# Performance work log

Measured on AMD Instinct MI355X. Metric: run time of the kernel, lower is better.

Reference implementation:

```python
import jax, jax.numpy as jnp
import numpy as np
import math

D_MODEL = 1024
N_HEADS = 16
D_K = D_MODEL // N_HEADS
FFN = 4096
B, S = 4, 1024
EPS = 1e-5


def setup_inputs() -> dict:
    key = jax.random.key(0)
    ks = jax.random.split(key, 24)
    sd = 0.02
    def w(k, shape):
        return jax.random.normal(k, shape, dtype=jnp.float32) * sd
    inp = {
        'x': jax.random.normal(ks[0], (B, S, D_MODEL), dtype=jnp.float32),
        'enc': jax.random.normal(ks[1], (B, S, D_MODEL), dtype=jnp.float32),
        'mask': jnp.tril(jnp.ones((S, S), dtype=jnp.int32)),  # causal look-ahead mask
        # stacked per-head projections [H, d_model, d_k], biases [H, d_k]
        'Wq_self': w(ks[2], (N_HEADS, D_MODEL, D_K)), 'bq_self': w(ks[3], (N_HEADS, D_K)),
        'Wk_self': w(ks[4], (N_HEADS, D_MODEL, D_K)), 'bk_self': w(ks[5], (N_HEADS, D_K)),
        'Wv_self': w(ks[6], (N_HEADS, D_MODEL, D_K)), 'bv_self': w(ks[7], (N_HEADS, D_K)),
        'Wq_x': w(ks[8], (N_HEADS, D_MODEL, D_K)), 'bq_x': w(ks[9], (N_HEADS, D_K)),
        'Wk_x': w(ks[10], (N_HEADS, D_MODEL, D_K)), 'bk_x': w(ks[11], (N_HEADS, D_K)),
        'Wv_x': w(ks[12], (N_HEADS, D_MODEL, D_K)), 'bv_x': w(ks[13], (N_HEADS, D_K)),
        # W_O is SHARED between self- and cross-attention (as in the torch code)
        'Wo': w(ks[14], (D_MODEL, D_MODEL)), 'bo': w(ks[15], (D_MODEL,)),
        'W1': w(ks[16], (D_MODEL, FFN)), 'b1': w(ks[17], (FFN,)),
        'W2': w(ks[18], (FFN, D_MODEL)), 'b2': w(ks[19], (D_MODEL,)),
        'g1': jnp.ones((D_MODEL,), jnp.float32), 'be1': jnp.zeros((D_MODEL,), jnp.float32),
        'g2': jnp.ones((D_MODEL,), jnp.float32), 'be2': jnp.zeros((D_MODEL,), jnp.float32),
        'g3': jnp.ones((D_MODEL,), jnp.float32), 'be3': jnp.zeros((D_MODEL,), jnp.float32),
    }
    return inp


def _layernorm(x, g, b):
    mu = jnp.mean(x, axis=-1, keepdims=True)
    d = x - mu
    var = jnp.mean(d * d, axis=-1, keepdims=True)
    return d * jax.lax.rsqrt(var + EPS) * g + b


def _mha(xq, xkv, Wq, bq, Wk, bk, Wv, bv, mask):
    # batched equivalent of the per-head Python loop
    q = jnp.einsum('bsd,hdk->bhsk', xq, Wq) + bq[None, :, None, :]
    k = jnp.einsum('btd,hdk->bhtk', xkv, Wk) + bk[None, :, None, :]
    v = jnp.einsum('btd,hdk->bhtk', xkv, Wv) + bv[None, :, None, :]
    scores = jnp.einsum('bhsk,bhtk->bhst', q, k) / math.sqrt(D_K)
    if mask is not None:
        scores = jnp.where(mask[None, None] == 0, -jnp.inf, scores)
    attn = jax.nn.softmax(scores, axis=-1)
    z = jnp.einsum('bhst,bhtk->bhsk', attn, v)
    # concat heads along last dim (head i occupies slice i, matching torch.cat)
    b_, h_, s_, k_ = z.shape
    return jnp.transpose(z, (0, 2, 1, 3)).reshape(b_, s_, h_ * k_)


def reference(x, enc, mask, Wq_self, bq_self, Wk_self, bk_self, Wv_self, bv_self,
              Wq_x, bq_x, Wk_x, bk_x, Wv_x, bv_x, Wo, bo, W1, b1, W2, b2,
              g1, be1, g2, be2, g3, be3):
    sa = _mha(x, x, Wq_self, bq_self, Wk_self, bk_self, Wv_self, bv_self, mask)
    x1 = _layernorm(x + sa @ Wo + bo, g1, be1)
    ca = _mha(x1, enc, Wq_x, bq_x, Wk_x, bk_x, Wv_x, bv_x, None)
    x2 = _layernorm(x1 + ca @ Wo + bo, g2, be2)
    ffn = jax.nn.relu(x2 @ W1 + b1) @ W2 + b2
    return _layernorm(x2 + ffn, g3, be3)
```

## Files before the change

### kernel.cpp

```cpp
#include <hip/hip_runtime.h>
#include <cstdint>

typedef __bf16 bf16_t;
typedef bf16_t bf16x8 __attribute__((ext_vector_type(8)));
typedef bf16_t bf16x4 __attribute__((ext_vector_type(4)));
typedef float  f32x4  __attribute__((ext_vector_type(4)));

#define DEVI static __device__ __forceinline__

DEVI void async_ld16(const bf16_t* g, bf16_t* l) {
  __builtin_amdgcn_global_load_lds((const __attribute__((address_space(1))) void*)g,
                                   (__attribute__((address_space(3))) void*)l, 16, 0, 0);
}

struct PrepArgs {
  const float *WqS, *WkS, *WvS, *WqX, *WkX, *WvX, *Wo, *W1, *W2, *x, *enc;
  const float *bqS, *bkS, *bvS, *bkX, *bvX;
  bf16_t *WqkvST, *WqXT, *WkvXT, *WoT, *W1T, *W2T, *xb, *encb;
  float *bqkv, *bkvx;
};

__global__ __launch_bounds__(256)
void k_prep(PrepArgs a)
{
  __shared__ float tile[32][33];
  const int blk = blockIdx.x, tid = threadIdx.x;
  const int tx = tid & 31, ty = tid >> 5;

  const float* src = nullptr;
  bf16_t* dst = nullptr;
  int srcLd = 0, dstLd = 0, m0 = 0, n0 = 0;
  bool do_tr = false;

  if (blk < 6144) {
    int j = blk >> 10, q = blk & 1023;
    src = j == 0 ? a.WqS : j == 1 ? a.WkS : j == 2 ? a.WvS : j == 3 ? a.WqX : j == 4 ? a.WkX : a.WvX;
    dst = j == 0 ? a.WqkvST : j == 1 ? a.WqkvST + 1048576 : j == 2 ? a.WqkvST + 2097152
        : j == 3 ? a.WqXT : j == 4 ? a.WkvXT : a.WkvXT + 1048576;
    int batch = q >> 6, rem = q & 63;
    src += (long)batch * 65536; dst += (long)batch * 65536;
    srcLd = 64; dstLd = 1024;
    n0 = (rem & 1) * 32; m0 = (rem >> 1) * 32;
    do_tr = true;
  } else if (blk < 7168) {
    int q = blk - 6144;
    src = a.Wo; dst = a.WoT; srcLd = 1024; dstLd = 1024;
    m0 = (q >> 5) * 32; n0 = (q & 31) * 32; do_tr = true;
  } else if (blk < 11264) {
    int q = blk - 7168;
    src = a.W1; dst = a.W1T; srcLd = 4096; dstLd = 1024;
    m0 = (q >> 7) * 32; n0 = (q & 127) * 32; do_tr = true;
  } else if (blk < 15360) {
    int q = blk - 11264;
    src = a.W2; dst = a.W2T; srcLd = 1024; dstLd = 4096;
    m0 = (q >> 5) * 32; n0 = (q & 31) * 32; do_tr = true;
  } else if (blk < 16384) {
    long base = (long)(blk - 15360) * 4096 + tid * 4;
#pragma unroll
    for (int u = 0; u < 4; u++) {
      float4 v = *(const float4*)(a.x + base + u * 1024);
      bf16x4 o; o[0] = (bf16_t)v.x; o[1] = (bf16_t)v.y; o[2] = (bf16_t)v.z; o[3] = (bf16_t)v.w;
      *(bf16x4*)(a.xb + base + u * 1024) = o;
    }
    return;
  } else if (blk < 17408) {
    long base = (long)(blk - 16384) * 4096 + tid * 4;
#pragma unroll
    for (int u = 0; u < 4; u++) {
      float4 v = *(const float4*)(a.enc + base + u * 1024);
      bf16x4 o; o[0] = (bf16_t)v.x; o[1] = (bf16_t)v.y; o[2] = (bf16_t)v.z; o[3] = (bf16_t)v.w;
      *(bf16x4*)(a.encb + base + u * 1024) = o;
    }
    return;
  } else {
    int gi = (blk - 17408) * 1024 + tid * 4;
#pragma unroll
    for (int j = 0; j < 4; j++) {
      int i = gi + j;
      if (i < 1024)      a.bqkv[i] = a.bqS[i];
      else if (i < 2048) a.bqkv[i] = a.bkS[i - 1024];
      else if (i < 3072) a.bqkv[i] = a.bvS[i - 2048];
      else if (i < 4096) a.bkvx[i - 3072] = a.bkX[i - 3072];
      else if (i < 5120) a.bkvx[i - 3072] = a.bvX[i - 4096];
    }
    return;
  }

  if (do_tr) {
#pragma unroll
    for (int i = 0; i < 4; i++)
      tile[ty + i * 8][tx] = src[(long)(m0 + ty + i * 8) * srcLd + n0 + tx];
    __syncthreads();
#pragma unroll
    for (int i = 0; i < 4; i++)
      dst[(long)(n0 + ty + i * 8) * dstLd + m0 + tx] = (bf16_t)tile[tx][ty + i * 8];
  }
}

template<int OUT_MODE, int RELU, int VOFF>
__global__ __launch_bounds__(256, 2)
void k_gemm(const bf16_t* __restrict__ A, int lda,
            const bf16_t* __restrict__ Bt, int ldb,
            const float* __restrict__ bias,
            bf16_t* __restrict__ C, int ldc,
            bf16_t* __restrict__ Vt,
            bf16_t* __restrict__ p0, bf16_t* __restrict__ p1,
            bf16_t* __restrict__ p2, bf16_t* __restrict__ p3,
            int Ktot, int nx)
{
  __shared__ bf16_t As[2][128 * 32];
  __shared__ bf16_t Bs[2][128 * 32];
  const int tid  = threadIdx.x;
  const int wave = tid >> 6, lane = tid & 63;
  const int quad = lane >> 4, m16 = lane & 15;

  int lin = blockIdx.x;
  int perx = gridDim.x >> 3;
  int t = (lin & 7) * perx + (lin >> 3);
  const int bcol = (t % nx) * 128, brow = (t / nx) * 128;
  const int wr = (wave >> 1) * 64, wc = (wave & 1) * 64;

  const int Kper = Ktot / gridDim.z;
  const int k0 = blockIdx.z * Kper;

  f32x4 acc[4][4];
#pragma unroll
  for (int i = 0; i < 4; i++)
#pragma unroll
    for (int j = 0; j < 4; j++) acc[i][j] = (f32x4){0.f, 0.f, 0.f, 0.f};

  auto stage = [&](int kt, int buf) {
#pragma unroll
    for (int i = 0; i < 2; i++) {
      int rg = wave * 2 + i;
      async_ld16(A  + (long)(brow + rg * 16 + m16) * lda + kt + quad * 8, As[buf] + rg * 512);
      async_ld16(Bt + (long)(bcol + rg * 16 + m16) * ldb + kt + quad * 8, Bs[buf] + rg * 512);
    }
  };

  stage(k0, 0);
  __syncthreads();

  const int nIter = Kper >> 5;
  for (int it = 0; it < nIter; it++) {
    const int cur = it & 1;
    if (it + 1 < nIter) stage(k0 + (it + 1) * 32, cur ^ 1);

    bf16x8 af[4], bfr[4];
#pragma unroll
    for (int tt = 0; tt < 4; tt++) {
      af[tt]  = *(const bf16x8*)(As[cur] + ((wr + tt * 16) >> 4) * 512 + quad * 128 + m16 * 8);
      bfr[tt] = *(const bf16x8*)(Bs[cur] + ((wc + tt * 16) >> 4) * 512 + quad * 128 + m16 * 8);
    }
#pragma unroll
    for (int i = 0; i < 4; i++)
#pragma unroll
      for (int j = 0; j < 4; j++)
        acc[i][j] = __builtin_amdgcn_mfma_f32_16x16x32_bf16(af[i], bfr[j], acc[i][j], 0, 0, 0);

    __syncthreads();
  }

  if (OUT_MODE == 1) {
    bf16_t* P = blockIdx.z == 0 ? p0 : blockIdx.z == 1 ? p1 : blockIdx.z == 2 ? p2 : p3;
#pragma unroll
    for (int i = 0; i < 4; i++)
#pragma unroll
      for (int j = 0; j < 4; j++) {
        int col = bcol + wc + j * 16 + m16;
#pragma unroll
        for (int r = 0; r < 4; r++) {
          int row = brow + wr + i * 16 + quad * 4 + r;
          P[(long)row * ldc + col] = (bf16_t)acc[i][j][r];
        }
      }
  } else {
#pragma unroll
    for (int i = 0; i < 4; i++)
#pragma unroll
      for (int j = 0; j < 4; j++) {
        int col = bcol + wc + j * 16 + m16;
        float bv = bias[col];
        if (VOFF && col >= VOFF) {
          int hh = (col - VOFF) >> 6, dd = col & 63;
          int row0 = brow + wr + i * 16 + quad * 4;
          int bb = row0 >> 10, seq = row0 & 1023;
          bf16x4 pk;
#pragma unroll
          for (int r = 0; r < 4; r++) pk[r] = (bf16_t)(acc[i][j][r] + bv);
          *(bf16x4*)(Vt + (long)(bb * 16 + hh) * 65536 + dd * 1024 + seq) = pk;
        } else {
#pragma unroll
          for (int r = 0; r < 4; r++) {
            int row = brow + wr + i * 16 + quad * 4 + r;
            float v = acc[i][j][r] + bv;
            if (RELU) v = v > 0.f ? v : 0.f;
            C[(long)row * ldc + col] = (bf16_t)v;
          }
        }
      }
  }
}

template<int LN, int RESID, int OUTF, int OUTB>
__global__ __launch_bounds__(256)
void k_reduce4(const bf16_t* __restrict__ p0, const bf16_t* __restrict__ p1,
               const bf16_t* __restrict__ p2, const bf16_t* __restrict__ p3,
               const float* __restrict__ bias, const float* __restrict__ resid,
               const float* __restrict__ gamma, const float* __restrict__ beta,
               float* __restrict__ outf, bf16_t* __restrict__ outb)
{
  constexpr int D = 1024;
  __shared__ float red[8];
  int row = blockIdx.x, tid = threadIdx.x;
  long off = (long)row * D + tid * 4;
  bf16x4 a0 = *(const bf16x4*)(p0 + off);
  bf16x4 a1 = *(const bf16x4*)(p1 + off);
  bf16x4 a2 = *(const bf16x4*)(p2 + off);
  bf16x4 a3 = *(const bf16x4*)(p3 + off);
  float4 bb4 = *(const float4*)(bias + tid * 4);
  float4 v;
  v.x = (float)a0[0] + (float)a1[0] + (float)a2[0] + (float)a3[0] + bb4.x;
  v.y = (float)a0[1] + (float)a1[1] + (float)a2[1] + (float)a3[1] + bb4.y;
  v.z = (float)a0[2] + (float)a1[2] + (float)a2[2] + (float)a3[2] + bb4.z;
  v.w = (float)a0[3] + (float)a1[3] + (float)a2[3] + (float)a3[3] + bb4.w;
  if (RESID) {
    float4 q = *(const float4*)(resid + off);
    v.x += q.x; v.y += q.y; v.z += q.z; v.w += q.w;
  }
  float4 y = v;
  if (LN) {
    float s  = v.x + v.y + v.z + v.w;
    float sq = v.x * v.x + v.y * v.y + v.z * v.z + v.w * v.w;
#pragma unroll
    for (int o = 1; o < 64; o <<= 1) {
      s  += __shfl_xor(s, o, 64);
      sq += __shfl_xor(sq, o, 64);
    }
    int wave = tid >> 6, lane = tid & 63;
    if (lane == 0) { red[wave * 2] = s; red[wave * 2 + 1] = sq; }
    __syncthreads();
    float ts = red[0] + red[2] + red[4] + red[6];
    float tq = red[1] + red[3] + red[5] + red[7];
    float mu = ts * (1.f / D);
    float var = tq * (1.f / D) - mu * mu;
    float rstd = rsqrtf(var + 1e-5f);
    float4 g  = *(const float4*)(gamma + tid * 4);
    float4 be = *(const float4*)(beta + tid * 4);
    y.x = (v.x - mu) * rstd * g.x + be.x;
    y.y = (v.y - mu) * rstd * g.y + be.y;
    y.z = (v.z - mu) * rstd * g.z + be.z;
    y.w = (v.w - mu) * rstd * g.w + be.w;
  }
  if (OUTF) *(float4*)(outf + off) = y;
  if (OUTB) {
    bf16x4 o;
    o[0] = (bf16_t)y.x; o[1] = (bf16_t)y.y; o[2] = (bf16_t)y.z; o[3] = (bf16_t)y.w;
    *(bf16x4*)(outb + off) = o;
  }
}

template<int CAUSAL>
__global__ __launch_bounds__(256, 2)
void k_attn(const bf16_t* __restrict__ Q, int ldq,
            const bf16_t* __restrict__ Kp, int ldk,
            const bf16_t* __restrict__ Vt,
            bf16_t* __restrict__ O)
{
  constexpr int S = 1024;
  __shared__ bf16_t Kls[2][4096];
  __shared__ bf16_t Vls[2][4096];
  __shared__ bf16_t Pls[4][32 * 72];

  const int tid = threadIdx.x;
  const int wave = tid >> 6, lane = tid & 63;
  const int quad = lane >> 4, m16 = lane & 15;
  const int qt = blockIdx.x, bh = blockIdx.y, b = bh >> 4, h = bh & 15;
  const int qbase = qt * 128 + wave * 32;

  bf16x8 qf[2][2];
#pragma unroll
  for (int rh = 0; rh < 2; rh++) {
    const bf16_t* qp = Q + (long)(b * S + qbase + rh * 16 + m16) * ldq + h * 64 + quad * 8;
    qf[rh][0] = *(const bf16x8*)qp;
    qf[rh][1] = *(const bf16x8*)(qp + 32);
  }

  f32x4 o_acc[2][4];
#pragma unroll
  for (int rh = 0; rh < 2; rh++)
#pragma unroll
    for (int t = 0; t < 4; t++) o_acc[rh][t] = (f32x4){0.f, 0.f, 0.f, 0.f};
  float rsum[2][4];
#pragma unroll
  for (int rh = 0; rh < 2; rh++)
#pragma unroll
    for (int r = 0; r < 4; r++) rsum[rh][r] = 0.f;

  auto stage = [&](int c, int buf) {
#pragma unroll
    for (int i = 0; i < 2; i++) {
      int t2 = wave * 2 + i;
      int rg = t2 & 3, ph = t2 >> 2;
      async_ld16(Kp + (long)(b * S + c * 64 + rg * 16 + m16) * ldk + h * 64 + ph * 32 + quad * 8,
                 Kls[buf] + t2 * 512);
      async_ld16(Vt + (long)bh * 65536 + (rg * 16 + m16) * 1024 + c * 64 + ph * 32 + quad * 8,
                 Vls[buf] + t2 * 512);
    }
  };

  const int nch = CAUSAL ? (2 * qt + 2) : 16;
  stage(0, 0);

  for (int c = 0; c < nch; c++) {
    __syncthreads();
    const int cur = c & 1;
    if (c + 1 < nch) stage(c + 1, cur ^ 1);

    f32x4 s[2][4];
#pragma unroll
    for (int t = 0; t < 4; t++) {
      bf16x8 k0 = *(const bf16x8*)(Kls[cur] + (0 * 4 + t) * 512 + quad * 128 + m16 * 8);
      bf16x8 k1 = *(const bf16x8*)(Kls[cur] + (1 * 4 + t) * 512 + quad * 128 + m16 * 8);
#pragma unroll
      for (int rh = 0; rh < 2; rh++) {
        f32x4 z = (f32x4){0.f, 0.f, 0.f, 0.f};
        z = __builtin_amdgcn_mfma_f32_16x16x32_bf16(qf[rh][0], k0, z, 0, 0, 0);
        z = __builtin_amdgcn_mfma_f32_16x16x32_bf16(qf[rh][1], k1, z, 0, 0, 0);
        s[rh][t] = z;
      }
    }

    bf16_t* pw = Pls[wave];
#pragma unroll
    for (int rh = 0; rh < 2; rh++)
#pragma unroll
      for (int r = 0; r < 4; r++) {
        int qg = qbase + rh * 16 + quad * 4 + r;
#pragma unroll
        for (int t = 0; t < 4; t++) {
          float v = s[rh][t][r] * 0.125f;
          float p;
          if (CAUSAL) {
            int kvg = c * 64 + t * 16 + m16;
            p = (kvg <= qg) ? __expf(v) : 0.f;
          } else {
            p = __expf(v);
          }
          rsum[rh][r] += p;
          pw[(rh * 16 + quad * 4 + r) * 72 + t * 16 + m16] = (bf16_t)p;
        }
      }

    bf16x8 pf[2][2];
#pragma unroll
    for (int rh = 0; rh < 2; rh++)
#pragma unroll
      for (int kvh = 0; kvh < 2; kvh++)
        pf[rh][kvh] = *(const bf16x8*)(pw + (rh * 16 + m16) * 72 + kvh * 32 + quad * 8);
#pragma unroll
    for (int t = 0; t < 4; t++) {
      bf16x8 v0 = *(const bf16x8*)(Vls[cur] + (0 * 4 + t) * 512 + quad * 128 + m16 * 8);
      bf16x8 v1 = *(const bf16x8*)(Vls[cur] + (1 * 4 + t) * 512 + quad * 128 + m16 * 8);
#pragma unroll
      for (int rh = 0; rh < 2; rh++) {
        o_acc[rh][t] = __builtin_amdgcn_mfma_f32_16x16x32_bf16(pf[rh][0], v0, o_acc[rh][t], 0, 0, 0);
        o_acc[rh][t] = __builtin_amdgcn_mfma_f32_16x16x32_bf16(pf[rh][1], v1, o_acc[rh][t], 0, 0, 0);
      }
    }
  }

#pragma unroll
  for (int rh = 0; rh < 2; rh++)
#pragma unroll
    for (int r = 0; r < 4; r++) {
      float v = rsum[rh][r];
      v += __shfl_xor(v, 1, 64);
      v += __shfl_xor(v, 2, 64);
      v += __shfl_xor(v, 4, 64);
      v += __shfl_xor(v, 8, 64);
      rsum[rh][r] = 1.f / v;
    }
#pragma unroll
  for (int rh = 0; rh < 2; rh++)
#pragma unroll
    for (int t = 0; t < 4; t++)
#pragma unroll
      for (int r = 0; r < 4; r++) {
        int row = b * S + qbase + rh * 16 + quad * 4 + r;
        int col = h * 64 + t * 16 + m16;
        O[(long)row * 1024 + col] = (bf16_t)(o_acc[rh][t][r] * rsum[rh][r]);
      }
}

extern "C" void kernel_launch(void* const* d_in, const int* in_sizes, int n_in,
                              void* d_out, int out_size, void* d_ws, size_t ws_size,
                              hipStream_t stream)
{
  const float* x   = (const float*)d_in[0];
  const float* enc = (const float*)d_in[1];
  const float* WqS = (const float*)d_in[3];
  const float* bqS = (const float*)d_in[4];
  const float* WkS = (const float*)d_in[5];
  const float* bkS = (const float*)d_in[6];
  const float* WvS = (const float*)d_in[7];
  const float* bvS = (const float*)d_in[8];
  const float* WqX = (const float*)d_in[9];
  const float* bqX = (const float*)d_in[10];
  const float* WkX = (const float*)d_in[11];
  const float* bkX = (const float*)d_in[12];
  const float* WvX = (const float*)d_in[13];
  const float* bvX = (const float*)d_in[14];
  const float* Wo  = (const float*)d_in[15];
  const float* bo  = (const float*)d_in[16];
  const float* W1  = (const float*)d_in[17];
  const float* b1  = (const float*)d_in[18];
  const float* W2  = (const float*)d_in[19];
  const float* b2  = (const float*)d_in[20];
  const float* g1  = (const float*)d_in[21];
  const float* be1 = (const float*)d_in[22];
  const float* g2  = (const float*)d_in[23];
  const float* be2 = (const float*)d_in[24];
  const float* g3  = (const float*)d_in[25];
  const float* be3 = (const float*)d_in[26];

  char* ws = (char*)d_ws;
  const long MBy = 1048576;
  bf16_t* WqkvST = (bf16_t*)(ws + 0 * MBy);
  bf16_t* WqXT   = (bf16_t*)(ws + 6 * MBy);
  bf16_t* WkvXT  = (bf16_t*)(ws + 8 * MBy);
  bf16_t* WoT    = (bf16_t*)(ws + 12 * MBy);
  bf16_t* W1T    = (bf16_t*)(ws + 14 * MBy);
  bf16_t* W2T    = (bf16_t*)(ws + 22 * MBy);
  float*  bqkvS  = (float*)(ws + 30 * MBy);
  float*  bkvX   = (float*)(ws + 30 * MBy + 16384);
  bf16_t* xb     = (bf16_t*)(ws + 31 * MBy);
  bf16_t* Qx     = xb;
  bf16_t* encb   = (bf16_t*)(ws + 39 * MBy);
  float*  x1f    = (float*)(ws + 47 * MBy);
  bf16_t* x1b    = (bf16_t*)(ws + 63 * MBy);
  bf16_t* Z      = (bf16_t*)(ws + 71 * MBy);
  bf16_t* QK     = (bf16_t*)(ws + 79 * MBy);
  bf16_t* Kenc   = (bf16_t*)(ws + 79 * MBy);
  bf16_t* Vt     = (bf16_t*)(ws + 95 * MBy);
  bf16_t* pa0 = (bf16_t*)(ws + 95 * MBy);
  bf16_t* pa1 = (bf16_t*)(ws + 103 * MBy);
  bf16_t* pa2 = (bf16_t*)(ws + 111 * MBy);
  bf16_t* pa3 = (bf16_t*)(ws + 119 * MBy);
  bf16_t* Hbuf = (bf16_t*)(ws + 95 * MBy);
  bf16_t* pf0 = (bf16_t*)(ws + 0 * MBy);
  bf16_t* pf1 = (bf16_t*)(ws + 8 * MBy);
  bf16_t* pf2 = (bf16_t*)(ws + 31 * MBy);
  bf16_t* pf3 = (bf16_t*)(ws + 39 * MBy);

  dim3 tb(256);

  PrepArgs pa;
  pa.WqS = WqS; pa.WkS = WkS; pa.WvS = WvS; pa.WqX = WqX; pa.WkX = WkX; pa.WvX = WvX;
  pa.Wo = Wo; pa.W1 = W1; pa.W2 = W2; pa.x = x; pa.enc = enc;
  pa.bqS = bqS; pa.bkS = bkS; pa.bvS = bvS; pa.bkX = bkX; pa.bvX = bvX;
  pa.WqkvST = WqkvST; pa.WqXT = WqXT; pa.WkvXT = WkvXT; pa.WoT = WoT;
  pa.W1T = W1T; pa.W2T = W2T; pa.xb = xb; pa.encb = encb;
  pa.bqkv = bqkvS; pa.bkvx = bkvX;
  k_prep<<<dim3(17413), tb, 0, stream>>>(pa);

  k_gemm<0, 0, 2048><<<dim3(768, 1, 1), tb, 0, stream>>>(
      xb, 1024, WqkvST, 1024, bqkvS, QK, 2048, Vt,
      nullptr, nullptr, nullptr, nullptr, 1024, 24);
  k_attn<1><<<dim3(8, 64), tb, 0, stream>>>(QK, 2048, QK + 1024, 2048, Vt, Z);
  k_gemm<1, 0, 0><<<dim3(256, 1, 4), tb, 0, stream>>>(
      Z, 1024, WoT, 1024, nullptr, nullptr, 1024, nullptr,
      pa0, pa1, pa2, pa3, 1024, 8);
  k_reduce4<1, 1, 1, 1><<<dim3(4096), tb, 0, stream>>>(
      pa0, pa1, pa2, pa3, bo, x, g1, be1, x1f, x1b);

  k_gemm<1, 0, 0><<<dim3(256, 1, 4), tb, 0, stream>>>(
      x1b, 1024, WqXT, 1024, nullptr, nullptr, 1024, nullptr,
      pa0, pa1, pa2, pa3, 1024, 8);
  k_reduce4<0, 0, 0, 1><<<dim3(4096), tb, 0, stream>>>(
      pa0, pa1, pa2, pa3, bqX, nullptr, nullptr, nullptr, nullptr, Qx);
  k_gemm<0, 0, 1024><<<dim3(512, 1, 1), tb, 0, stream>>>(
      encb, 1024, WkvXT, 1024, bkvX, Kenc, 1024, Vt,
      nullptr, nullptr, nullptr, nullptr, 1024, 16);
  k_attn<0><<<dim3(8, 64), tb, 0, stream>>>(Qx, 1024, Kenc, 1024, Vt, Z);
  k_gemm<1, 0, 0><<<dim3(256, 1, 4), tb, 0, stream>>>(
      Z, 1024, WoT, 1024, nullptr, nullptr, 1024, nullptr,
      pa0, pa1, pa2, pa3, 1024, 8);
  k_reduce4<1, 1, 1, 1><<<dim3(4096), tb, 0, stream>>>(
      pa0, pa1, pa2, pa3, bo, x1f, g2, be2, x1f, x1b);

  k_gemm<0, 1, 0><<<dim3(1024, 1, 1), tb, 0, stream>>>(
      x1b, 1024, W1T, 1024, b1, Hbuf, 4096, nullptr,
      nullptr, nullptr, nullptr, nullptr, 1024, 32);
  k_gemm<1, 0, 0><<<dim3(256, 1, 4), tb, 0, stream>>>(
      Hbuf, 4096, W2T, 4096, nullptr, nullptr, 1024, nullptr,
      pf0, pf1, pf2, pf3, 4096, 8);
  k_reduce4<1, 1, 1, 0><<<dim3(4096), tb, 0, stream>>>(
      pf0, pf1, pf2, pf3, b2, x1f, g3, be3, (float*)d_out, nullptr);
}
```

Baseline: 596.3 us.

## Replace split-K N=1024 GEMMs with 64x64-tile full-K GEMM and drop partial reductions

Adds a 64x64-tile bf16 MFMA GEMM that runs over the full K dimension with a bias epilogue. It replaces the 4-way split-K GEMMs and their four-partial reduce kernels for the output projections, the cross-attention Q projection and FFN2. The aim is to stop writing and re-reading four bf16 partial buffers. The Q projection also no longer needs a separate reduce kernel. In exchange the small tiles give less data reuse per block and longer serial K loops (4096 for FFN2), using only a double-buffered 32-wide K stage.

```diff
diff --git a/kernel.cpp b/kernel.cpp
--- a/kernel.cpp
+++ b/kernel.cpp
@@ -202,56 +202,117 @@
   }
 }
 
-template<int LN, int RESID, int OUTF, int OUTB>
+template<int RELU>
+__global__ __launch_bounds__(256, 4)
+void k_gemm64(const bf16_t* __restrict__ A, int lda,
+              const bf16_t* __restrict__ Bt, int ldb,
+              const float* __restrict__ bias,
+              bf16_t* __restrict__ C, int ldc,
+              int Ktot, int nx)
+{
+  __shared__ bf16_t As[2][64 * 32];
+  __shared__ bf16_t Bs[2][64 * 32];
+  const int tid  = threadIdx.x;
+  const int wave = tid >> 6, lane = tid & 63;
+  const int quad = lane >> 4, m16 = lane & 15;
+  const int wr = wave >> 1, wc = wave & 1;
+
+  int lin = blockIdx.x;
+  int perx = gridDim.x >> 3;
+  int t = (lin & 7) * perx + (lin >> 3);
+  const int bcol = (t % nx) * 64, brow = (t / nx) * 64;
+
+  f32x4 acc[2][2];
+#pragma unroll
+  for (int i = 0; i < 2; i++)
+#pragma unroll
+    for (int j = 0; j < 2; j++) acc[i][j] = (f32x4){0.f, 0.f, 0.f, 0.f};
+
+  auto stage = [&](int kt, int buf) {
+    async_ld16(A  + (long)(brow + wave * 16 + m16) * lda + kt + quad * 8, As[buf] + wave * 512);
+    async_ld16(Bt + (long)(bcol + wave * 16 + m16) * ldb + kt + quad * 8, Bs[buf] + wave * 512);
+  };
+
+  stage(0, 0);
+  __syncthreads();
+
+  const int nIter = Ktot >> 5;
+  for (int it = 0; it < nIter; it++) {
+    const int cur = it & 1;
+    if (it + 1 < nIter) stage((it + 1) * 32, cur ^ 1);
+
+    bf16x8 af[2], bfr[2];
+#pragma unroll
+    for (int tt = 0; tt < 2; tt++) {
+      af[tt]  = *(const bf16x8*)(As[cur] + (wr * 2 + tt) * 512 + quad * 128 + m16 * 8);
+      bfr[tt] = *(const bf16x8*)(Bs[cur] + (wc * 2 + tt) * 512 + quad * 128 + m16 * 8);
+    }
+#pragma unroll
+    for (int i = 0; i < 2; i++)
+#pragma unroll
+      for (int j = 0; j < 2; j++)
+        acc[i][j] = __builtin_amdgcn_mfma_f32_16x16x32_bf16(af[i], bfr[j], acc[i][j], 0, 0, 0);
+
+    __syncthreads();
+  }
+
+#pragma unroll
+  for (int i = 0; i < 2; i++)
+#pragma unroll
+    for (int j = 0; j < 2; j++) {
+      int col = bcol + wc * 32 + j * 16 + m16;
+      float bv = bias[col];
+#pragma unroll
+      for (int r = 0; r < 4; r++) {
+        int row = brow + wr * 32 + i * 16 + quad * 4 + r;
+        float v = acc[i][j][r] + bv;
+        if (RELU) v = v > 0.f ? v : 0.f;
+        C[(long)row * ldc + col] = (bf16_t)v;
+      }
+    }
+}
+
+template<int OUTF, int OUTB>
 __global__ __launch_bounds__(256)
-void k_reduce4(const bf16_t* __restrict__ p0, const bf16_t* __restrict__ p1,
-               const bf16_t* __restrict__ p2, const bf16_t* __restrict__ p3,
-               const float* __restrict__ bias, const float* __restrict__ resid,
-               const float* __restrict__ gamma, const float* __restrict__ beta,
-               float* __restrict__ outf, bf16_t* __restrict__ outb)
+void k_post(const bf16_t* __restrict__ C, const float* __restrict__ resid,
+            const float* __restrict__ gamma, const float* __restrict__ beta,
+            float* __restrict__ outf, bf16_t* __restrict__ outb)
 {
   constexpr int D = 1024;
   __shared__ float red[8];
   int row = blockIdx.x, tid = threadIdx.x;
   long off = (long)row * D + tid * 4;
-  bf16x4 a0 = *(const bf16x4*)(p0 + off);
-  bf16x4 a1 = *(const bf16x4*)(p1 + off);
-  bf16x4 a2 = *(const bf16x4*)(p2 + off);
-  bf16x4 a3 = *(const bf16x4*)(p3 + off);
-  float4 bb4 = *(const float4*)(bias + tid * 4);
+  bf16x4 a0 = *(const bf16x4*)(C + off);
+  float4 q = *(const float4*)(resid + off);
   float4 v;
-  v.x = (float)a0[0] + (float)a1[0] + (float)a2[0] + (float)a3[0] + bb4.x;
-  v.y = (float)a0[1] + (float)a1[1] + (float)a2[1] + (float)a3[1] + bb4.y;
-  v.z = (float)a0[2] + (float)a1[2] + (float)a2[2] + (float)a3[2] + bb4.z;
-  v.w = (float)a0[3] + (float)a1[3] + (float)a2[3] + (float)a3[3] + bb4.w;
-  if (RESID) {
-    float4 q = *(const float4*)(resid + off);
-    v.x += q.x; v.y += q.y; v.z += q.z; v.w += q.w;
-  }
-  float4 y = v;
-  if (LN) {
-    float s  = v.x + v.y + v.z + v.w;
-    float sq = v.x * v.x + v.y * v.y + v.z * v.z + v.w * v.w;
-#pragma unroll
-    for (int o = 1; o < 64; o <<= 1) {
-      s  += __shfl_xor(s, o, 64);
-      sq += __shfl_xor(sq, o, 64);
-    }
-    int wave = tid >> 6, lane = tid & 63;
-    if (lane == 0) { red[wave * 2] = s; red[wave * 2 + 1] = sq; }
-    __syncthreads();
-    float ts = red[0] + red[2] + red[4] + red[6];
-    float tq = red[1] + red[3] + red[5] + red[7];
-    float mu = ts * (1.f / D);
-    float var = tq * (1.f / D) - mu * mu;
-    float rstd = rsqrtf(var + 1e-5f);
-    float4 g  = *(const float4*)(gamma + tid * 4);
-    float4 be = *(const float4*)(beta + tid * 4);
-    y.x = (v.x - mu) * rstd * g.x + be.x;
-    y.y = (v.y - mu) * rstd * g.y + be.y;
-    y.z = (v.z - mu) * rstd * g.z + be.z;
-    y.w = (v.w - mu) * rstd * g.w + be.w;
-  }
+  v.x = (float)a0[0] + q.x;
+  v.y = (float)a0[1] + q.y;
+  v.z = (float)a0[2] + q.z;
+  v.w = (float)a0[3] + q.w;
+
+  float s  = v.x + v.y + v.z + v.w;
+  float sq = v.x * v.x + v.y * v.y + v.z * v.z + v.w * v.w;
+#pragma unroll
+  for (int o = 1; o < 64; o <<= 1) {
+    s  += __shfl_xor(s, o, 64);
+    sq += __shfl_xor(sq, o, 64);
+  }
+  int wave = tid >> 6, lane = tid & 63;
+  if (lane == 0) { red[wave * 2] = s; red[wave * 2 + 1] = sq; }
+  __syncthreads();
+  float ts = red[0] + red[2] + red[4] + red[6];
+  float tq = red[1] + red[3] + red[5] + red[7];
+  float mu = ts * (1.f / D);
+  float var = tq * (1.f / D) - mu * mu;
+  float rstd = rsqrtf(var + 1e-5f);
+  float4 g  = *(const float4*)(gamma + tid * 4);
+  float4 be = *(const float4*)(beta + tid * 4);
+  float4 y;
+  y.x = (v.x - mu) * rstd * g.x + be.x;
+  y.y = (v.y - mu) * rstd * g.y + be.y;
+  y.z = (v.z - mu) * rstd * g.z + be.z;
+  y.w = (v.w - mu) * rstd * g.w + be.w;
+
   if (OUTF) *(float4*)(outf + off) = y;
   if (OUTB) {
     bf16x4 o;
@@ -443,15 +504,9 @@
   bf16_t* QK     = (bf16_t*)(ws + 79 * MBy);
   bf16_t* Kenc   = (bf16_t*)(ws + 79 * MBy);
   bf16_t* Vt     = (bf16_t*)(ws + 95 * MBy);
-  bf16_t* pa0 = (bf16_t*)(ws + 95 * MBy);
-  bf16_t* pa1 = (bf16_t*)(ws + 103 * MBy);
-  bf16_t* pa2 = (bf16_t*)(ws + 111 * MBy);
-  bf16_t* pa3 = (bf16_t*)(ws + 119 * MBy);
-  bf16_t* Hbuf = (bf16_t*)(ws + 95 * MBy);
-  bf16_t* pf0 = (bf16_t*)(ws + 0 * MBy);
-  bf16_t* pf1 = (bf16_t*)(ws + 8 * MBy);
-  bf16_t* pf2 = (bf16_t*)(ws + 31 * MBy);
-  bf16_t* pf3 = (bf16_t*)(ws + 39 * MBy);
+  bf16_t* Cw     = (bf16_t*)(ws + 95 * MBy);
+  bf16_t* Hbuf   = (bf16_t*)(ws + 95 * MBy);
+  bf16_t* Cw2    = (bf16_t*)(ws + 0 * MBy);
 
   dim3 tb(256);
 
@@ -468,33 +523,24 @@
       xb, 1024, WqkvST, 1024, bqkvS, QK, 2048, Vt,
       nullptr, nullptr, nullptr, nullptr, 1024, 24);
   k_attn<1><<<dim3(8, 64), tb, 0, stream>>>(QK, 2048, QK + 1024, 2048, Vt, Z);
-  k_gemm<1, 0, 0><<<dim3(256, 1, 4), tb, 0, stream>>>(
-      Z, 1024, WoT, 1024, nullptr, nullptr, 1024, nullptr,
-      pa0, pa1, pa2, pa3, 1024, 8);
-  k_reduce4<1, 1, 1, 1><<<dim3(4096), tb, 0, stream>>>(
-      pa0, pa1, pa2, pa3, bo, x, g1, be1, x1f, x1b);
-
-  k_gemm<1, 0, 0><<<dim3(256, 1, 4), tb, 0, stream>>>(
-      x1b, 1024, WqXT, 1024, nullptr, nullptr, 1024, nullptr,
-      pa0, pa1, pa2, pa3, 1024, 8);
-  k_reduce4<0, 0, 0, 1><<<dim3(4096), tb, 0, stream>>>(
-      pa0, pa1, pa2, pa3, bqX, nullptr, nullptr, nullptr, nullptr, Qx);
+  k_gemm64<0><<<dim3(1024), tb, 0, stream>>>(
+      Z, 1024, WoT, 1024, bo, Cw, 1024, 1024, 16);
+  k_post<1, 1><<<dim3(4096), tb, 0, stream>>>(Cw, x, g1, be1, x1f, x1b);
+
+  k_gemm64<0><<<dim3(1024), tb, 0, stream>>>(
+      x1b, 1024, WqXT, 1024, bqX, Qx, 1024, 1024, 16);
   k_gemm<0, 0, 1024><<<dim3(512, 1, 1), tb, 0, stream>>>(
       encb, 1024, WkvXT, 1024, bkvX, Kenc, 1024, Vt,
       nullptr, nullptr, nullptr, nullptr, 1024, 16);
   k_attn<0><<<dim3(8, 64), tb, 0, stream>>>(Qx, 1024, Kenc, 1024, Vt, Z);
-  k_gemm<1, 0, 0><<<dim3(256, 1, 4), tb, 0, stream>>>(
-      Z, 1024, WoT, 1024, nullptr, nullptr, 1024, nullptr,
-      pa0, pa1, pa2, pa3, 1024, 8);
-  k_reduce4<1, 1, 1, 1><<<dim3(4096), tb, 0, stream>>>(
-      pa0, pa1, pa2, pa3, bo, x1f, g2, be2, x1f, x1b);
+  k_gemm64<0><<<dim3(1024), tb, 0, stream>>>(
+      Z, 1024, WoT, 1024, bo, Cw, 1024, 1024, 16);
+  k_post<1, 1><<<dim3(4096), tb, 0, stream>>>(Cw, x1f, g2, be2, x1f, x1b);
 
   k_gemm<0, 1, 0><<<dim3(1024, 1, 1), tb, 0, stream>>>(
       x1b, 1024, W1T, 1024, b1, Hbuf, 4096, nullptr,
       nullptr, nullptr, nullptr, nullptr, 1024, 32);
-  k_gemm<1, 0, 0><<<dim3(256, 1, 4), tb, 0, stream>>>(
-      Hbuf, 4096, W2T, 4096, nullptr, nullptr, 1024, nullptr,
-      pf0, pf1, pf2, pf3, 4096, 8);
-  k_reduce4<1, 1, 1, 0><<<dim3(4096), tb, 0, stream>>>(
-      pf0, pf1, pf2, pf3, b2, x1f, g3, be3, (float*)d_out, nullptr);
-}
+  k_gemm64<0><<<dim3(1024), tb, 0, stream>>>(
+      Hbuf, 4096, W2T, 4096, b2, Cw2, 1024, 4096, 16);
+  k_post<1, 0><<<dim3(4096), tb, 0, stream>>>(Cw2, x1f, g3, be3, (float*)d_out, nullptr);
+}
```

After: 646.8 us. 8.5% more time.

## Load attention K/V fragments directly from global memory, drop LDS staging

Applied to the files above, without the earlier changes.

Removes the double-buffered LDS staging of K and V tiles and the per-chunk __syncthreads in the attention kernel. Each wave now reads its K and V MFMA operands straight from global memory, relying on L1/L2 for the reuse across the four waves. It also raises wave priority around the MFMA blocks. The cost is about four times more global/L2 traffic per block and no software prefetch, so load latency is exposed unless occupancy hides it.

```diff
diff --git a/kernel.cpp b/kernel.cpp
--- a/kernel.cpp
+++ b/kernel.cpp
@@ -268,8 +268,6 @@
             bf16_t* __restrict__ O)
 {
   constexpr int S = 1024;
-  __shared__ bf16_t Kls[2][4096];
-  __shared__ bf16_t Vls[2][4096];
   __shared__ bf16_t Pls[4][32 * 72];
 
   const int tid = threadIdx.x;
@@ -286,6 +284,9 @@
     qf[rh][1] = *(const bf16x8*)(qp + 32);
   }
 
+  const bf16_t* Kbase = Kp + (long)(b * S + m16) * ldk + h * 64 + quad * 8;
+  const bf16_t* Vbase = Vt + (long)bh * 65536 + (long)m16 * 1024 + quad * 8;
+
   f32x4 o_acc[2][4];
 #pragma unroll
   for (int rh = 0; rh < 2; rh++)
@@ -297,31 +298,16 @@
 #pragma unroll
     for (int r = 0; r < 4; r++) rsum[rh][r] = 0.f;
 
-  auto stage = [&](int c, int buf) {
-#pragma unroll
-    for (int i = 0; i < 2; i++) {
-      int t2 = wave * 2 + i;
-      int rg = t2 & 3, ph = t2 >> 2;
-      async_ld16(Kp + (long)(b * S + c * 64 + rg * 16 + m16) * ldk + h * 64 + ph * 32 + quad * 8,
-                 Kls[buf] + t2 * 512);
-      async_ld16(Vt + (long)bh * 65536 + (rg * 16 + m16) * 1024 + c * 64 + ph * 32 + quad * 8,
-                 Vls[buf] + t2 * 512);
-    }
-  };
-
   const int nch = CAUSAL ? (2 * qt + 2) : 16;
-  stage(0, 0);
 
   for (int c = 0; c < nch; c++) {
-    __syncthreads();
-    const int cur = c & 1;
-    if (c + 1 < nch) stage(c + 1, cur ^ 1);
-
     f32x4 s[2][4];
 #pragma unroll
     for (int t = 0; t < 4; t++) {
-      bf16x8 k0 = *(const bf16x8*)(Kls[cur] + (0 * 4 + t) * 512 + quad * 128 + m16 * 8);
-      bf16x8 k1 = *(const bf16x8*)(Kls[cur] + (1 * 4 + t) * 512 + quad * 128 + m16 * 8);
+      const bf16_t* kp = Kbase + (long)(c * 64 + t * 16) * ldk;
+      bf16x8 k0 = *(const bf16x8*)kp;
+      bf16x8 k1 = *(const bf16x8*)(kp + 32);
+      __builtin_amdgcn_s_setprio(1);
 #pragma unroll
       for (int rh = 0; rh < 2; rh++) {
         f32x4 z = (f32x4){0.f, 0.f, 0.f, 0.f};
@@ -329,6 +315,7 @@
         z = __builtin_amdgcn_mfma_f32_16x16x32_bf16(qf[rh][1], k1, z, 0, 0, 0);
         s[rh][t] = z;
       }
+      __builtin_amdgcn_s_setprio(0);
     }
 
     bf16_t* pw = Pls[wave];
@@ -360,13 +347,16 @@
         pf[rh][kvh] = *(const bf16x8*)(pw + (rh * 16 + m16) * 72 + kvh * 32 + quad * 8);
 #pragma unroll
     for (int t = 0; t < 4; t++) {
-      bf16x8 v0 = *(const bf16x8*)(Vls[cur] + (0 * 4 + t) * 512 + quad * 128 + m16 * 8);
-      bf16x8 v1 = *(const bf16x8*)(Vls[cur] + (1 * 4 + t) * 512 + quad * 128 + m16 * 8);
+      const bf16_t* vp = Vbase + (long)t * 16384 + c * 64;
+      bf16x8 v0 = *(const bf16x8*)vp;
+      bf16x8 v1 = *(const bf16x8*)(vp + 32);
+      __builtin_amdgcn_s_setprio(1);
 #pragma unroll
       for (int rh = 0; rh < 2; rh++) {
         o_acc[rh][t] = __builtin_amdgcn_mfma_f32_16x16x32_bf16(pf[rh][0], v0, o_acc[rh][t], 0, 0, 0);
         o_acc[rh][t] = __builtin_amdgcn_mfma_f32_16x16x32_bf16(pf[rh][1], v1, o_acc[rh][t], 0, 0, 0);
       }
+      __builtin_amdgcn_s_setprio(0);
     }
   }
 
```

New measurement: 655.4 us. +9.9%, slower.

## Add 256x256-tile 512-thread GEMM for big projections and halve split-K

Applied to the files above, without the earlier changes.

Adds a new GEMM kernel with 256x256 output tiles, 512 threads and double-buffered async LDS loads, and uses it for the fused QKV projection, FFN1 and FFN2. This raises arithmetic intensity per block and cuts global traffic for the large GEMMs. The Wo and cross-Q projections drop from 4-way to 2-way split-K, and the reduce kernel is templated on the number of partials, so less partial-sum traffic is written and read. The cost is fewer blocks in flight (192, 256 or 256 blocks on a 256-CU part), heavy register pressure from a 128-float accumulator per thread, and 64KB of LDS per block, which may limit occupancy and latency hiding.

```diff
diff --git a/kernel.cpp b/kernel.cpp
--- a/kernel.cpp
+++ b/kernel.cpp
@@ -202,9 +202,115 @@
   }
 }
 
-template<int LN, int RESID, int OUTF, int OUTB>
+template<int OUT_MODE, int RELU, int VOFF>
+__global__ __launch_bounds__(512, 4)
+void k_gemm256(const bf16_t* __restrict__ A, int lda,
+               const bf16_t* __restrict__ Bt, int ldb,
+               const float* __restrict__ bias,
+               bf16_t* __restrict__ C, int ldc,
+               bf16_t* __restrict__ Vt,
+               bf16_t* __restrict__ p0, bf16_t* __restrict__ p1,
+               bf16_t* __restrict__ p2, bf16_t* __restrict__ p3,
+               int Ktot, int nx)
+{
+  __shared__ bf16_t As[2][256 * 32];
+  __shared__ bf16_t Bs[2][256 * 32];
+  const int tid  = threadIdx.x;
+  const int wave = tid >> 6, lane = tid & 63;
+  const int quad = lane >> 4, m16 = lane & 15;
+
+  int lin = blockIdx.x;
+  int perx = gridDim.x >> 3;
+  int t = (lin & 7) * perx + (lin >> 3);
+  const int bcol = (t % nx) * 256, brow = (t / nx) * 256;
+  const int wr = (wave >> 2) * 128, wc = (wave & 3) * 64;
+
+  const int Kper = Ktot / gridDim.z;
+  const int k0 = blockIdx.z * Kper;
+
+  f32x4 acc[8][4];
+#pragma unroll
+  for (int i = 0; i < 8; i++)
+#pragma unroll
+    for (int j = 0; j < 4; j++) acc[i][j] = (f32x4){0.f, 0.f, 0.f, 0.f};
+
+  auto stage = [&](int kt, int buf) {
+#pragma unroll
+    for (int i = 0; i < 2; i++) {
+      int rg = wave * 2 + i;
+      async_ld16(A  + (long)(brow + rg * 16 + m16) * lda + kt + quad * 8, As[buf] + rg * 512);
+      async_ld16(Bt + (long)(bcol + rg * 16 + m16) * ldb + kt + quad * 8, Bs[buf] + rg * 512);
+    }
+  };
+
+  stage(k0, 0);
+  __syncthreads();
+
+  const int nIter = Kper >> 5;
+  for (int it = 0; it < nIter; it++) {
+    const int cur = it & 1;
+    if (it + 1 < nIter) stage(k0 + (it + 1) * 32, cur ^ 1);
+
+    bf16x8 af[8], bfr[4];
+#pragma unroll
+    for (int tt = 0; tt < 8; tt++)
+      af[tt]  = *(const bf16x8*)(As[cur] + ((wr + tt * 16) >> 4) * 512 + quad * 128 + m16 * 8);
+#pragma unroll
+    for (int j = 0; j < 4; j++)
+      bfr[j] = *(const bf16x8*)(Bs[cur] + ((wc + j * 16) >> 4) * 512 + quad * 128 + m16 * 8);
+#pragma unroll
+    for (int i = 0; i < 8; i++)
+#pragma unroll
+      for (int j = 0; j < 4; j++)
+        acc[i][j] = __builtin_amdgcn_mfma_f32_16x16x32_bf16(af[i], bfr[j], acc[i][j], 0, 0, 0);
+
+    __syncthreads();
+  }
+
+  if (OUT_MODE == 1) {
+    bf16_t* P = blockIdx.z == 0 ? p0 : blockIdx.z == 1 ? p1 : blockIdx.z == 2 ? p2 : p3;
+#pragma unroll
+    for (int i = 0; i < 8; i++)
+#pragma unroll
+      for (int j = 0; j < 4; j++) {
+        int col = bcol + wc + j * 16 + m16;
+#pragma unroll
+        for (int r = 0; r < 4; r++) {
+          int row = brow + wr + i * 16 + quad * 4 + r;
+          P[(long)row * ldc + col] = (bf16_t)acc[i][j][r];
+        }
+      }
+  } else {
+#pragma unroll
+    for (int i = 0; i < 8; i++)
+#pragma unroll
+      for (int j = 0; j < 4; j++) {
+        int col = bcol + wc + j * 16 + m16;
+        float bv = bias[col];
+        if (VOFF && col >= VOFF) {
+          int hh = (col - VOFF) >> 6, dd = col & 63;
+          int row0 = brow + wr + i * 16 + quad * 4;
+          int bb = row0 >> 10, seq = row0 & 1023;
+          bf16x4 pk;
+#pragma unroll
+          for (int r = 0; r < 4; r++) pk[r] = (bf16_t)(acc[i][j][r] + bv);
+          *(bf16x4*)(Vt + (long)(bb * 16 + hh) * 65536 + dd * 1024 + seq) = pk;
+        } else {
+#pragma unroll
+          for (int r = 0; r < 4; r++) {
+            int row = brow + wr + i * 16 + quad * 4 + r;
+            float v = acc[i][j][r] + bv;
+            if (RELU) v = v > 0.f ? v : 0.f;
+            C[(long)row * ldc + col] = (bf16_t)v;
+          }
+        }
+      }
+  }
+}
+
+template<int LN, int RESID, int OUTF, int OUTB, int NPART>
 __global__ __launch_bounds__(256)
-void k_reduce4(const bf16_t* __restrict__ p0, const bf16_t* __restrict__ p1,
+void k_reduceN(const bf16_t* __restrict__ p0, const bf16_t* __restrict__ p1,
                const bf16_t* __restrict__ p2, const bf16_t* __restrict__ p3,
                const float* __restrict__ bias, const float* __restrict__ resid,
                const float* __restrict__ gamma, const float* __restrict__ beta,
@@ -216,14 +322,20 @@
   long off = (long)row * D + tid * 4;
   bf16x4 a0 = *(const bf16x4*)(p0 + off);
   bf16x4 a1 = *(const bf16x4*)(p1 + off);
-  bf16x4 a2 = *(const bf16x4*)(p2 + off);
-  bf16x4 a3 = *(const bf16x4*)(p3 + off);
   float4 bb4 = *(const float4*)(bias + tid * 4);
   float4 v;
-  v.x = (float)a0[0] + (float)a1[0] + (float)a2[0] + (float)a3[0] + bb4.x;
-  v.y = (float)a0[1] + (float)a1[1] + (float)a2[1] + (float)a3[1] + bb4.y;
-  v.z = (float)a0[2] + (float)a1[2] + (float)a2[2] + (float)a3[2] + bb4.z;
-  v.w = (float)a0[3] + (float)a1[3] + (float)a2[3] + (float)a3[3] + bb4.w;
+  v.x = (float)a0[0] + (float)a1[0] + bb4.x;
+  v.y = (float)a0[1] + (float)a1[1] + bb4.y;
+  v.z = (float)a0[2] + (float)a1[2] + bb4.z;
+  v.w = (float)a0[3] + (float)a1[3] + bb4.w;
+  if (NPART == 4) {
+    bf16x4 a2 = *(const bf16x4*)(p2 + off);
+    bf16x4 a3 = *(const bf16x4*)(p3 + off);
+    v.x += (float)a2[0] + (float)a3[0];
+    v.y += (float)a2[1] + (float)a3[1];
+    v.z += (float)a2[2] + (float)a3[2];
+    v.w += (float)a2[3] + (float)a3[3];
+  }
   if (RESID) {
     float4 q = *(const float4*)(resid + off);
     v.x += q.x; v.y += q.y; v.z += q.z; v.w += q.w;
@@ -445,15 +557,13 @@
   bf16_t* Vt     = (bf16_t*)(ws + 95 * MBy);
   bf16_t* pa0 = (bf16_t*)(ws + 95 * MBy);
   bf16_t* pa1 = (bf16_t*)(ws + 103 * MBy);
-  bf16_t* pa2 = (bf16_t*)(ws + 111 * MBy);
-  bf16_t* pa3 = (bf16_t*)(ws + 119 * MBy);
   bf16_t* Hbuf = (bf16_t*)(ws + 95 * MBy);
   bf16_t* pf0 = (bf16_t*)(ws + 0 * MBy);
   bf16_t* pf1 = (bf16_t*)(ws + 8 * MBy);
   bf16_t* pf2 = (bf16_t*)(ws + 31 * MBy);
   bf16_t* pf3 = (bf16_t*)(ws + 39 * MBy);
 
-  dim3 tb(256);
+  dim3 tb(256), tb512(512);
 
   PrepArgs pa;
   pa.WqS = WqS; pa.WkS = WkS; pa.WvS = WvS; pa.WqX = WqX; pa.WkX = WkX; pa.WvX = WvX;
@@ -464,37 +574,37 @@
   pa.bqkv = bqkvS; pa.bkvx = bkvX;
   k_prep<<<dim3(17413), tb, 0, stream>>>(pa);
 
-  k_gemm<0, 0, 2048><<<dim3(768, 1, 1), tb, 0, stream>>>(
+  k_gemm256<0, 0, 2048><<<dim3(192, 1, 1), tb512, 0, stream>>>(
       xb, 1024, WqkvST, 1024, bqkvS, QK, 2048, Vt,
-      nullptr, nullptr, nullptr, nullptr, 1024, 24);
+      nullptr, nullptr, nullptr, nullptr, 1024, 12);
   k_attn<1><<<dim3(8, 64), tb, 0, stream>>>(QK, 2048, QK + 1024, 2048, Vt, Z);
-  k_gemm<1, 0, 0><<<dim3(256, 1, 4), tb, 0, stream>>>(
+  k_gemm<1, 0, 0><<<dim3(256, 1, 2), tb, 0, stream>>>(
       Z, 1024, WoT, 1024, nullptr, nullptr, 1024, nullptr,
-      pa0, pa1, pa2, pa3, 1024, 8);
-  k_reduce4<1, 1, 1, 1><<<dim3(4096), tb, 0, stream>>>(
-      pa0, pa1, pa2, pa3, bo, x, g1, be1, x1f, x1b);
-
-  k_gemm<1, 0, 0><<<dim3(256, 1, 4), tb, 0, stream>>>(
+      pa0, pa1, nullptr, nullptr, 1024, 8);
+  k_reduceN<1, 1, 1, 1, 2><<<dim3(4096), tb, 0, stream>>>(
+      pa0, pa1, nullptr, nullptr, bo, x, g1, be1, x1f, x1b);
+
+  k_gemm<1, 0, 0><<<dim3(256, 1, 2), tb, 0, stream>>>(
       x1b, 1024, WqXT, 1024, nullptr, nullptr, 1024, nullptr,
-      pa0, pa1, pa2, pa3, 1024, 8);
-  k_reduce4<0, 0, 0, 1><<<dim3(4096), tb, 0, stream>>>(
-      pa0, pa1, pa2, pa3, bqX, nullptr, nullptr, nullptr, nullptr, Qx);
+      pa0, pa1, nullptr, nullptr, 1024, 8);
+  k_reduceN<0, 0, 0, 1, 2><<<dim3(4096), tb, 0, stream>>>(
+      pa0, pa1, nullptr, nullptr, bqX, nullptr, nullptr, nullptr, nullptr, Qx);
   k_gemm<0, 0, 1024><<<dim3(512, 1, 1), tb, 0, stream>>>(
       encb, 1024, WkvXT, 1024, bkvX, Kenc, 1024, Vt,
       nullptr, nullptr, nullptr, nullptr, 1024, 16);
   k_attn<0><<<dim3(8, 64), tb, 0, stream>>>(Qx, 1024, Kenc, 1024, Vt, Z);
-  k_gemm<1, 0, 0><<<dim3(256, 1, 4), tb, 0, stream>>>(
+  k_gemm<1, 0, 0><<<dim3(256, 1, 2), tb, 0, stream>>>(
       Z, 1024, WoT, 1024, nullptr, nullptr, 1024, nullptr,
-      pa0, pa1, pa2, pa3, 1024, 8);
-  k_reduce4<1, 1, 1, 1><<<dim3(4096), tb, 0, stream>>>(
-      pa0, pa1, pa2, pa3, bo, x1f, g2, be2, x1f, x1b);
-
-  k_gemm<0, 1, 0><<<dim3(1024, 1, 1), tb, 0, stream>>>(
+      pa0, pa1, nullptr, nullptr, 1024, 8);
+  k_reduceN<1, 1, 1, 1, 2><<<dim3(4096), tb, 0, stream>>>(
+      pa0, pa1, nullptr, nullptr, bo, x1f, g2, be2, x1f, x1b);
+
+  k_gemm256<0, 1, 0><<<dim3(256, 1, 1), tb512, 0, stream>>>(
       x1b, 1024, W1T, 1024, b1, Hbuf, 4096, nullptr,
-      nullptr, nullptr, nullptr, nullptr, 1024, 32);
-  k_gemm<1, 0, 0><<<dim3(256, 1, 4), tb, 0, stream>>>(
+      nullptr, nullptr, nullptr, nullptr, 1024, 16);
+  k_gemm256<1, 0, 0><<<dim3(64, 1, 4), tb512, 0, stream>>>(
       Hbuf, 4096, W2T, 4096, nullptr, nullptr, 1024, nullptr,
-      pf0, pf1, pf2, pf3, 4096, 8);
-  k_reduce4<1, 1, 1, 0><<<dim3(4096), tb, 0, stream>>>(
+      pf0, pf1, pf2, pf3, 4096, 4);
+  k_reduceN<1, 1, 1, 0, 4><<<dim3(4096), tb, 0, stream>>>(
       pf0, pf1, pf2, pf3, b2, x1f, g3, be3, (float*)d_out, nullptr);
 }
```

New measurement: 928.2 us. 1.56x slower.
